# Optimization experiments

Hardware: AMD Instinct MI355X
Metric: run time of the kernel (lower is better)

## Reference

```python
import jax, jax.numpy as jnp
import numpy as np

LN_EPS = 1e-6  # flax nn.LayerNorm default epsilon
NEG_SLOPE = 0.01  # jax.nn.leaky_relu default


def _layer_norm(x, scale, bias):
    m = jnp.mean(x, axis=-1, keepdims=True)
    v = jnp.mean(jnp.square(x - m), axis=-1, keepdims=True)
    return (x - m) * jax.lax.rsqrt(v + LN_EPS) * scale + bias


def setup_inputs() -> dict:
    key = jax.random.key(0)
    ks = jax.random.split(key, 10)
    B, D1, D2, OUT = 32768, 1024, 512, 1024
    inp = {
        "x1": jax.random.normal(ks[0], (B, D1), dtype=jnp.float32),
        "x2": jax.random.normal(ks[1], (B, D2), dtype=jnp.float32),
        # LayerNorm params (one per stream)
        "ln_scale1": jnp.ones((D1,), jnp.float32),
        "ln_bias1": jnp.zeros((D1,), jnp.float32),
        "ln_scale2": jnp.ones((D2,), jnp.float32),
        "ln_bias2": jnp.zeros((D2,), jnp.float32),
        # output Dense per stream: Dense(output_size)
        "W_out1": jax.random.normal(ks[2], (D1, OUT), jnp.float32) / np.sqrt(D1),
        "b_out1": jnp.zeros((OUT,), jnp.float32),
        "W_out2": jax.random.normal(ks[3], (D2, OUT), jnp.float32) / np.sqrt(D2),
        "b_out2": jnp.zeros((OUT,), jnp.float32),
        # gate Dense per stream: Dense(gate_size=output_size) for POINTWISE
        "W_g1": jax.random.normal(ks[4], (D1, OUT), jnp.float32) / np.sqrt(D1),
        "b_g1": jnp.zeros((OUT,), jnp.float32),
        "W_g2": jax.random.normal(ks[5], (D2, OUT), jnp.float32) / np.sqrt(D2),
        "b_g2": jnp.zeros((OUT,), jnp.float32),
    }
    return inp


def reference(x1, x2, ln_scale1, ln_bias1, ln_scale2, ln_bias2,
              W_out1, b_out1, W_out2, b_out2,
              W_g1, b_g1, W_g2, b_g2):
    # per-stream: LayerNorm -> leaky_relu -> Dense(output_size); pre-Dense
    # activation is also fed to the gate Dense.
    f1 = jax.nn.leaky_relu(_layer_norm(x1, ln_scale1, ln_bias1), NEG_SLOPE)
    f2 = jax.nn.leaky_relu(_layer_norm(x2, ln_scale2, ln_bias2), NEG_SLOPE)
    out1 = f1 @ W_out1 + b_out1  # [B, OUT]
    out2 = f2 @ W_out2 + b_out2  # [B, OUT]
    # two-stream POINTWISE gate: sum of gate Denses, sigmoid; the original
    # broadcasts gate [B,OUT] over stack([out1,out2]) and sums axis 0,
    # i.e. output = gate * (out1 + out2).
    gate = jax.nn.sigmoid((f1 @ W_g1 + b_g1) + (f2 @ W_g2 + b_g2))
    return gate * (out1 + out2)
```

## Files before the change

### kernel.cpp

```cpp
#include <hip/hip_runtime.h>
#include <hip/hip_bf16.h>
#include <stdint.h>

typedef __bf16 bf16x8 __attribute__((ext_vector_type(8)));
typedef float floatx4 __attribute__((ext_vector_type(4)));

__device__ __forceinline__ ushort f2bf(float f) {
  union { float f; uint32_t u; } v; v.f = f;
  uint32_t r = (v.u + 0x7fffu + ((v.u >> 16) & 1u)) >> 16;
  return (ushort)r;
}

__device__ __forceinline__ void load_lds16(const ushort* g, ushort* l) {
  __builtin_amdgcn_global_load_lds(
      (__attribute__((address_space(1))) void*)g,
      (__attribute__((address_space(3))) void*)l, 16, 0, 0);
}

__global__ __launch_bounds__(256) void ln2_kernel(
    const float* __restrict__ x1, const float* __restrict__ x2,
    const float* __restrict__ sc1p, const float* __restrict__ bi1p,
    const float* __restrict__ sc2p, const float* __restrict__ bi2p,
    ushort* __restrict__ f) {
  const int row = blockIdx.x;
  const int t = threadIdx.x;
  const float4 v1 = ((const float4*)(x1 + (size_t)row * 1024))[t];
  const float2 v2 = ((const float2*)(x2 + (size_t)row * 512))[t];
  float s1 = v1.x + v1.y + v1.z + v1.w;
  float q1 = v1.x * v1.x + v1.y * v1.y + v1.z * v1.z + v1.w * v1.w;
  float s2 = v2.x + v2.y;
  float q2 = v2.x * v2.x + v2.y * v2.y;
#pragma unroll
  for (int o = 32; o > 0; o >>= 1) {
    s1 += __shfl_down(s1, o);
    q1 += __shfl_down(q1, o);
    s2 += __shfl_down(s2, o);
    q2 += __shfl_down(q2, o);
  }
  __shared__ float red[4][4];
  const int wave = t >> 6, lane = t & 63;
  if (lane == 0) { red[0][wave] = s1; red[1][wave] = q1; red[2][wave] = s2; red[3][wave] = q2; }
  __syncthreads();
  s1 = 0.f; q1 = 0.f; s2 = 0.f; q2 = 0.f;
#pragma unroll
  for (int i = 0; i < 4; i++) { s1 += red[0][i]; q1 += red[1][i]; s2 += red[2][i]; q2 += red[3][i]; }
  const float m1 = s1 * (1.0f / 1024.0f);
  const float r1 = rsqrtf(q1 * (1.0f / 1024.0f) - m1 * m1 + 1e-6f);
  const float m2 = s2 * (1.0f / 512.0f);
  const float r2 = rsqrtf(q2 * (1.0f / 512.0f) - m2 * m2 + 1e-6f);
  const float4 sc1 = ((const float4*)sc1p)[t];
  const float4 bi1 = ((const float4*)bi1p)[t];
  const float2 sc2 = ((const float2*)sc2p)[t];
  const float2 bi2 = ((const float2*)bi2p)[t];
  float y0 = (v1.x - m1) * r1 * sc1.x + bi1.x;
  float y1 = (v1.y - m1) * r1 * sc1.y + bi1.y;
  float y2 = (v1.z - m1) * r1 * sc1.z + bi1.z;
  float y3 = (v1.w - m1) * r1 * sc1.w + bi1.w;
  float z0 = (v2.x - m2) * r2 * sc2.x + bi2.x;
  float z1 = (v2.y - m2) * r2 * sc2.y + bi2.y;
  y0 = y0 >= 0.f ? y0 : 0.01f * y0;
  y1 = y1 >= 0.f ? y1 : 0.01f * y1;
  y2 = y2 >= 0.f ? y2 : 0.01f * y2;
  y3 = y3 >= 0.f ? y3 : 0.01f * y3;
  z0 = z0 >= 0.f ? z0 : 0.01f * z0;
  z1 = z1 >= 0.f ? z1 : 0.01f * z1;
  ushort* frow = f + (size_t)row * 1536;
  ushort4 o1; o1.x = f2bf(y0); o1.y = f2bf(y1); o1.z = f2bf(y2); o1.w = f2bf(y3);
  ((ushort4*)frow)[t] = o1;
  ushort2 o2; o2.x = f2bf(z0); o2.y = f2bf(z1);
  ((ushort2*)(frow + 1024))[t] = o2;
}

__global__ __launch_bounds__(256) void wprep_kernel(
    const float* __restrict__ Wo1, const float* __restrict__ Wo2,
    const float* __restrict__ Wg1, const float* __restrict__ Wg2,
    ushort* __restrict__ WT) {
  __shared__ float tile[32][33];
  const int k0 = blockIdx.x * 32;
  const int j0 = blockIdx.y * 32;
  const int s = blockIdx.z;
  const float* Wa = s ? Wg1 : Wo1;
  const float* Wb = s ? Wg2 : Wo2;
  const int tx = threadIdx.x;
  const int ty = threadIdx.y;
#pragma unroll
  for (int r = 0; r < 4; r++) {
    const int k = k0 + ty + 8 * r;
    const float val = (k < 1024) ? Wa[(size_t)k * 1024 + j0 + tx]
                                 : Wb[(size_t)(k - 1024) * 1024 + j0 + tx];
    tile[ty + 8 * r][tx] = val;
  }
  __syncthreads();
#pragma unroll
  for (int r = 0; r < 4; r++) {
    const int j = j0 + ty + 8 * r;
    const int c = j & 63;
    const int n = (j >> 6) * 128 + (c >> 5) * 64 + s * 32 + ((c >> 4) & 1) * 16 + (c & 15);
    WT[(size_t)n * 1536 + k0 + tx] = f2bf(tile[tx][ty + 8 * r]);
  }
}

__global__ __launch_bounds__(256) void gemm_fused(
    const ushort* __restrict__ A,
    const ushort* __restrict__ Bt,
    const float* __restrict__ bo1, const float* __restrict__ bo2,
    const float* __restrict__ bg1, const float* __restrict__ bg2,
    float* __restrict__ out) {
  __shared__ __align__(16) ushort As[128 * 32];
  __shared__ __align__(16) ushort Bs[128 * 32];
  const int nt = blockIdx.x;
  const int mt = blockIdx.y;
  const int tid = threadIdx.x;
  const int wave = tid >> 6, lane = tid & 63;
  const int wr = wave >> 1, wc = wave & 1;
  const int quad = lane >> 4, low = lane & 15;

  const size_t arow0 = (size_t)mt * 128;
  const size_t brow0 = (size_t)nt * 128;

  const int r0 = tid >> 2;
  const int cc = (tid & 3) ^ ((r0 + (tid >> 4)) & 3);
  const ushort* gA = A + (arow0 + r0) * 1536 + cc * 8;
  const ushort* gB = Bt + (brow0 + r0) * 1536 + cc * 8;
  ushort* lA = &As[wave * 512];
  ushort* lB = &Bs[wave * 512];

  const ushort* pA[4];
  const ushort* pB[4];
#pragma unroll
  for (int i = 0; i < 4; i++) {
    const int rA = wr * 64 + i * 16 + low;
    pA[i] = &As[rA * 32 + (quad ^ ((rA + (rA >> 2)) & 3)) * 8];
    const int rB = wc * 64 + i * 16 + low;
    pB[i] = &Bs[rB * 32 + (quad ^ ((rB + (rB >> 2)) & 3)) * 8];
  }

  floatx4 acc[4][4];
#pragma unroll
  for (int i = 0; i < 4; i++)
#pragma unroll
    for (int j = 0; j < 4; j++) acc[i][j] = (floatx4)0.0f;

  for (int kt = 0; kt < 48; kt++) {
    const ushort* a = gA + kt * 32;
    const ushort* b = gB + kt * 32;
    load_lds16(a, lA);
    load_lds16(a + 64 * 1536, lA + 256 * 8);
    load_lds16(b, lB);
    load_lds16(b + 64 * 1536, lB + 256 * 8);
    __syncthreads();
    bf16x8 af[4], bfr[4];
#pragma unroll
    for (int i = 0; i < 4; i++) af[i] = *(const bf16x8*)pA[i];
#pragma unroll
    for (int j = 0; j < 4; j++) bfr[j] = *(const bf16x8*)pB[j];
#pragma unroll
    for (int i = 0; i < 4; i++)
#pragma unroll
      for (int j = 0; j < 4; j++)
        acc[i][j] = __builtin_amdgcn_mfma_f32_16x16x32_bf16(af[i], bfr[j], acc[i][j], 0, 0, 0);
    __syncthreads();
  }

#pragma unroll
  for (int jt = 0; jt < 2; jt++) {
    const int col = nt * 64 + wc * 32 + jt * 16 + low;
    const float bs = bo1[col] + bo2[col];
    const float bgv = bg1[col] + bg2[col];
#pragma unroll
    for (int i = 0; i < 4; i++) {
      const floatx4 S = acc[i][jt];
      const floatx4 G = acc[i][jt + 2];
      const size_t rb = (size_t)mt * 128 + wr * 64 + i * 16 + quad * 4;
#pragma unroll
      for (int r = 0; r < 4; r++) {
        const float sv = S[r] + bs;
        const float gv = G[r] + bgv;
        const float gate = 1.0f / (1.0f + __expf(-gv));
        out[(rb + r) * 1024 + col] = gate * sv;
      }
    }
  }
}

extern "C" void kernel_launch(void* const* d_in, const int* in_sizes, int n_in,
                              void* d_out, int out_size, void* d_ws, size_t ws_size,
                              hipStream_t stream) {
  const float* x1 = (const float*)d_in[0];
  const float* x2 = (const float*)d_in[1];
  const float* ln_s1 = (const float*)d_in[2];
  const float* ln_b1 = (const float*)d_in[3];
  const float* ln_s2 = (const float*)d_in[4];
  const float* ln_b2 = (const float*)d_in[5];
  const float* W_out1 = (const float*)d_in[6];
  const float* b_out1 = (const float*)d_in[7];
  const float* W_out2 = (const float*)d_in[8];
  const float* b_out2 = (const float*)d_in[9];
  const float* W_g1 = (const float*)d_in[10];
  const float* b_g1 = (const float*)d_in[11];
  const float* W_g2 = (const float*)d_in[12];
  const float* b_g2 = (const float*)d_in[13];
  float* out = (float*)d_out;

  ushort* f = (ushort*)d_ws;
  ushort* WT = f + (size_t)32768 * 1536;

  ln2_kernel<<<32768, 256, 0, stream>>>(x1, x2, ln_s1, ln_b1, ln_s2, ln_b2, f);
  wprep_kernel<<<dim3(48, 32, 2), dim3(32, 8), 0, stream>>>(W_out1, W_out2, W_g1, W_g2, WT);
  gemm_fused<<<dim3(16, 256), 256, 0, stream>>>(f, WT, b_out1, b_out2, b_g1, b_g2, out);
}
```

Baseline: 538.5 us.

## Use 256x256 double-buffered GEMM tiles with 8 waves and one-wave-per-row LayerNorm

The GEMM moves from 128x128 tiles with 4 waves and a single LDS buffer to 256x256 tiles with 8 waves, K-steps of 64, and double-buffered LDS. Loads for the next tile are staged between MFMA phases, and the kernel adds barrier and setprio interleaving plus a grid swizzle for L2 reuse. The goal is to overlap global loads with MFMA work and raise arithmetic intensity per LDS byte. The LayerNorm kernel now handles one row per wave with an xor-shuffle reduction, which drops the block-level sync and LDS. In exchange, the GEMM uses 128 KB of LDS and more registers, which may limit occupancy.

```diff
diff --git a/kernel.cpp b/kernel.cpp
--- a/kernel.cpp
+++ b/kernel.cpp
@@ -16,59 +16,68 @@
       (__attribute__((address_space(1))) void*)g,
       (__attribute__((address_space(3))) void*)l, 16, 0, 0);
 }
+
+__device__ __forceinline__ float leaky(float x) { return x >= 0.f ? x : 0.01f * x; }
 
 __global__ __launch_bounds__(256) void ln2_kernel(
     const float* __restrict__ x1, const float* __restrict__ x2,
     const float* __restrict__ sc1p, const float* __restrict__ bi1p,
     const float* __restrict__ sc2p, const float* __restrict__ bi2p,
     ushort* __restrict__ f) {
-  const int row = blockIdx.x;
-  const int t = threadIdx.x;
-  const float4 v1 = ((const float4*)(x1 + (size_t)row * 1024))[t];
-  const float2 v2 = ((const float2*)(x2 + (size_t)row * 512))[t];
-  float s1 = v1.x + v1.y + v1.z + v1.w;
-  float q1 = v1.x * v1.x + v1.y * v1.y + v1.z * v1.z + v1.w * v1.w;
-  float s2 = v2.x + v2.y;
-  float q2 = v2.x * v2.x + v2.y * v2.y;
-#pragma unroll
-  for (int o = 32; o > 0; o >>= 1) {
-    s1 += __shfl_down(s1, o);
-    q1 += __shfl_down(q1, o);
-    s2 += __shfl_down(s2, o);
-    q2 += __shfl_down(q2, o);
-  }
-  __shared__ float red[4][4];
-  const int wave = t >> 6, lane = t & 63;
-  if (lane == 0) { red[0][wave] = s1; red[1][wave] = q1; red[2][wave] = s2; red[3][wave] = q2; }
-  __syncthreads();
-  s1 = 0.f; q1 = 0.f; s2 = 0.f; q2 = 0.f;
-#pragma unroll
-  for (int i = 0; i < 4; i++) { s1 += red[0][i]; q1 += red[1][i]; s2 += red[2][i]; q2 += red[3][i]; }
+  const int row = (blockIdx.x << 2) + (threadIdx.x >> 6);
+  const int lane = threadIdx.x & 63;
+  const float4* X1 = (const float4*)(x1 + (size_t)row * 1024);
+  const float4* X2 = (const float4*)(x2 + (size_t)row * 512);
+  float4 v1[4], v2[2];
+#pragma unroll
+  for (int j = 0; j < 4; j++) v1[j] = X1[j * 64 + lane];
+#pragma unroll
+  for (int j = 0; j < 2; j++) v2[j] = X2[j * 64 + lane];
+  float s1 = 0.f, q1 = 0.f, s2 = 0.f, q2 = 0.f;
+#pragma unroll
+  for (int j = 0; j < 4; j++) {
+    s1 += v1[j].x + v1[j].y + v1[j].z + v1[j].w;
+    q1 += v1[j].x * v1[j].x + v1[j].y * v1[j].y + v1[j].z * v1[j].z + v1[j].w * v1[j].w;
+  }
+#pragma unroll
+  for (int j = 0; j < 2; j++) {
+    s2 += v2[j].x + v2[j].y + v2[j].z + v2[j].w;
+    q2 += v2[j].x * v2[j].x + v2[j].y * v2[j].y + v2[j].z * v2[j].z + v2[j].w * v2[j].w;
+  }
+#pragma unroll
+  for (int o = 1; o < 64; o <<= 1) {
+    s1 += __shfl_xor(s1, o);
+    q1 += __shfl_xor(q1, o);
+    s2 += __shfl_xor(s2, o);
+    q2 += __shfl_xor(q2, o);
+  }
   const float m1 = s1 * (1.0f / 1024.0f);
   const float r1 = rsqrtf(q1 * (1.0f / 1024.0f) - m1 * m1 + 1e-6f);
   const float m2 = s2 * (1.0f / 512.0f);
   const float r2 = rsqrtf(q2 * (1.0f / 512.0f) - m2 * m2 + 1e-6f);
-  const float4 sc1 = ((const float4*)sc1p)[t];
-  const float4 bi1 = ((const float4*)bi1p)[t];
-  const float2 sc2 = ((const float2*)sc2p)[t];
-  const float2 bi2 = ((const float2*)bi2p)[t];
-  float y0 = (v1.x - m1) * r1 * sc1.x + bi1.x;
-  float y1 = (v1.y - m1) * r1 * sc1.y + bi1.y;
-  float y2 = (v1.z - m1) * r1 * sc1.z + bi1.z;
-  float y3 = (v1.w - m1) * r1 * sc1.w + bi1.w;
-  float z0 = (v2.x - m2) * r2 * sc2.x + bi2.x;
-  float z1 = (v2.y - m2) * r2 * sc2.y + bi2.y;
-  y0 = y0 >= 0.f ? y0 : 0.01f * y0;
-  y1 = y1 >= 0.f ? y1 : 0.01f * y1;
-  y2 = y2 >= 0.f ? y2 : 0.01f * y2;
-  y3 = y3 >= 0.f ? y3 : 0.01f * y3;
-  z0 = z0 >= 0.f ? z0 : 0.01f * z0;
-  z1 = z1 >= 0.f ? z1 : 0.01f * z1;
   ushort* frow = f + (size_t)row * 1536;
-  ushort4 o1; o1.x = f2bf(y0); o1.y = f2bf(y1); o1.z = f2bf(y2); o1.w = f2bf(y3);
-  ((ushort4*)frow)[t] = o1;
-  ushort2 o2; o2.x = f2bf(z0); o2.y = f2bf(z1);
-  ((ushort2*)(frow + 1024))[t] = o2;
+#pragma unroll
+  for (int j = 0; j < 4; j++) {
+    const float4 sc = ((const float4*)sc1p)[j * 64 + lane];
+    const float4 bi = ((const float4*)bi1p)[j * 64 + lane];
+    const float y0 = leaky((v1[j].x - m1) * r1 * sc.x + bi.x);
+    const float y1 = leaky((v1[j].y - m1) * r1 * sc.y + bi.y);
+    const float y2 = leaky((v1[j].z - m1) * r1 * sc.z + bi.z);
+    const float y3 = leaky((v1[j].w - m1) * r1 * sc.w + bi.w);
+    ushort4 o; o.x = f2bf(y0); o.y = f2bf(y1); o.z = f2bf(y2); o.w = f2bf(y3);
+    ((ushort4*)frow)[j * 64 + lane] = o;
+  }
+#pragma unroll
+  for (int j = 0; j < 2; j++) {
+    const float4 sc = ((const float4*)sc2p)[j * 64 + lane];
+    const float4 bi = ((const float4*)bi2p)[j * 64 + lane];
+    const float z0 = leaky((v2[j].x - m2) * r2 * sc.x + bi.x);
+    const float z1 = leaky((v2[j].y - m2) * r2 * sc.y + bi.y);
+    const float z2 = leaky((v2[j].z - m2) * r2 * sc.z + bi.z);
+    const float z3 = leaky((v2[j].w - m2) * r2 * sc.w + bi.w);
+    ushort4 o; o.x = f2bf(z0); o.y = f2bf(z1); o.z = f2bf(z2); o.w = f2bf(z3);
+    ((ushort4*)(frow + 1024))[j * 64 + lane] = o;
+  }
 }
 
 __global__ __launch_bounds__(256) void wprep_kernel(
@@ -100,82 +109,143 @@
   }
 }
 
-__global__ __launch_bounds__(256) void gemm_fused(
+__global__ __launch_bounds__(512, 2) void gemm_fused(
     const ushort* __restrict__ A,
     const ushort* __restrict__ Bt,
     const float* __restrict__ bo1, const float* __restrict__ bo2,
     const float* __restrict__ bg1, const float* __restrict__ bg2,
     float* __restrict__ out) {
-  __shared__ __align__(16) ushort As[128 * 32];
-  __shared__ __align__(16) ushort Bs[128 * 32];
-  const int nt = blockIdx.x;
-  const int mt = blockIdx.y;
+  __shared__ __align__(16) ushort As[2][16384];
+  __shared__ __align__(16) ushort Bs[2][16384];
+  const int orig = blockIdx.x;
+  const int swz = (orig & 7) * 128 + (orig >> 3);
+  const int mt = swz >> 3;
+  const int nt = swz & 7;
   const int tid = threadIdx.x;
   const int wave = tid >> 6, lane = tid & 63;
-  const int wr = wave >> 1, wc = wave & 1;
-  const int quad = lane >> 4, low = lane & 15;
-
-  const size_t arow0 = (size_t)mt * 128;
-  const size_t brow0 = (size_t)nt * 128;
-
-  const int r0 = tid >> 2;
-  const int cc = (tid & 3) ^ ((r0 + (tid >> 4)) & 3);
-  const ushort* gA = A + (arow0 + r0) * 1536 + cc * 8;
-  const ushort* gB = Bt + (brow0 + r0) * 1536 + cc * 8;
-  ushort* lA = &As[wave * 512];
-  ushort* lB = &Bs[wave * 512];
-
-  const ushort* pA[4];
-  const ushort* pB[4];
-#pragma unroll
-  for (int i = 0; i < 4; i++) {
-    const int rA = wr * 64 + i * 16 + low;
-    pA[i] = &As[rA * 32 + (quad ^ ((rA + (rA >> 2)) & 3)) * 8];
-    const int rB = wc * 64 + i * 16 + low;
-    pB[i] = &Bs[rB * 32 + (quad ^ ((rB + (rB >> 2)) & 3)) * 8];
-  }
-
-  floatx4 acc[4][4];
-#pragma unroll
-  for (int i = 0; i < 4; i++)
-#pragma unroll
-    for (int j = 0; j < 4; j++) acc[i][j] = (floatx4)0.0f;
-
-  for (int kt = 0; kt < 48; kt++) {
-    const ushort* a = gA + kt * 32;
-    const ushort* b = gB + kt * 32;
-    load_lds16(a, lA);
-    load_lds16(a + 64 * 1536, lA + 256 * 8);
-    load_lds16(b, lB);
-    load_lds16(b + 64 * 1536, lB + 256 * 8);
-    __syncthreads();
-    bf16x8 af[4], bfr[4];
-#pragma unroll
-    for (int i = 0; i < 4; i++) af[i] = *(const bf16x8*)pA[i];
-#pragma unroll
-    for (int j = 0; j < 4; j++) bfr[j] = *(const bf16x8*)pB[j];
-#pragma unroll
-    for (int i = 0; i < 4; i++)
-#pragma unroll
-      for (int j = 0; j < 4; j++)
-        acc[i][j] = __builtin_amdgcn_mfma_f32_16x16x32_bf16(af[i], bfr[j], acc[i][j], 0, 0, 0);
-    __syncthreads();
-  }
-
-#pragma unroll
-  for (int jt = 0; jt < 2; jt++) {
-    const int col = nt * 64 + wc * 32 + jt * 16 + low;
+  const int wr = wave >> 2, wcol = wave & 3;
+  const int low = lane & 15, quad = lane >> 4;
+
+  const int srow = wave * 8 + (lane >> 3);
+  const int schunk = (lane & 7) ^ (lane >> 3);
+  const ushort* gA0 = A + ((size_t)mt * 256 + srow) * 1536 + schunk * 8;
+  const ushort* gB0 = Bt + ((size_t)nt * 256 + srow) * 1536 + schunk * 8;
+
+  const int q2 = quad ^ (low & 3);
+  const int kx = (low >> 2) & 1;
+  const int offA_k0 = (wr * 128 + low) * 64 + (q2 + 4 * kx) * 8;
+  const int offA_k1 = (wr * 128 + low) * 64 + (q2 + 4 * (1 - kx)) * 8;
+  const int offB_k0 = (wcol * 64 + low) * 64 + (q2 + 4 * kx) * 8;
+  const int offB_k1 = (wcol * 64 + low) * 64 + (q2 + 4 * (1 - kx)) * 8;
+
+  floatx4 acc[8][4];
+#pragma unroll
+  for (int m = 0; m < 8; m++)
+#pragma unroll
+    for (int n = 0; n < 4; n++) acc[m][n] = (floatx4)0.0f;
+
+#define STAGE_A(BUF, KT) do { \
+    const ushort* s_ = gA0 + (KT) * 64; \
+    ushort* d_ = &As[BUF][wave * 512]; \
+    load_lds16(s_, d_); \
+    load_lds16(s_ + 64 * 1536, d_ + 4096); \
+    load_lds16(s_ + 128 * 1536, d_ + 8192); \
+    load_lds16(s_ + 192 * 1536, d_ + 12288); \
+  } while (0)
+#define STAGE_B(BUF, KT) do { \
+    const ushort* s_ = gB0 + (KT) * 64; \
+    ushort* d_ = &Bs[BUF][wave * 512]; \
+    load_lds16(s_, d_); \
+    load_lds16(s_ + 64 * 1536, d_ + 4096); \
+    load_lds16(s_ + 128 * 1536, d_ + 8192); \
+    load_lds16(s_ + 192 * 1536, d_ + 12288); \
+  } while (0)
+
+  STAGE_A(0, 0);
+  STAGE_B(0, 0);
+  asm volatile("s_waitcnt vmcnt(0)" ::: "memory");
+  __builtin_amdgcn_s_barrier();
+  asm volatile("" ::: "memory");
+
+#define TILE_STEP(CUR, T) do { \
+    const ushort* Ac = &As[CUR][0]; \
+    const ushort* Bc = &Bs[CUR][0]; \
+    const bool pf = (T) < 23; \
+    bf16x8 a[4], b[4]; \
+     \
+    _Pragma("unroll") for (int m = 0; m < 4; m++) a[m] = *(const bf16x8*)(Ac + offA_k0 + m * 1024); \
+    _Pragma("unroll") for (int n = 0; n < 4; n++) b[n] = *(const bf16x8*)(Bc + offB_k0 + n * 1024); \
+    if (pf) STAGE_A((CUR) ^ 1, (T) + 1); \
+    asm volatile("" ::: "memory"); \
+    __builtin_amdgcn_s_barrier(); \
+    __builtin_amdgcn_s_setprio(1); \
+    _Pragma("unroll") for (int m = 0; m < 4; m++) \
+      _Pragma("unroll") for (int n = 0; n < 4; n++) \
+        acc[m][n] = __builtin_amdgcn_mfma_f32_16x16x32_bf16(a[m], b[n], acc[m][n], 0, 0, 0); \
+    __builtin_amdgcn_s_setprio(0); \
+    asm volatile("" ::: "memory"); \
+    __builtin_amdgcn_s_barrier(); \
+     \
+    _Pragma("unroll") for (int m = 0; m < 4; m++) a[m] = *(const bf16x8*)(Ac + offA_k0 + (m + 4) * 1024); \
+    if (pf) STAGE_B((CUR) ^ 1, (T) + 1); \
+    asm volatile("" ::: "memory"); \
+    __builtin_amdgcn_s_barrier(); \
+    __builtin_amdgcn_s_setprio(1); \
+    _Pragma("unroll") for (int m = 0; m < 4; m++) \
+      _Pragma("unroll") for (int n = 0; n < 4; n++) \
+        acc[m + 4][n] = __builtin_amdgcn_mfma_f32_16x16x32_bf16(a[m], b[n], acc[m + 4][n], 0, 0, 0); \
+    __builtin_amdgcn_s_setprio(0); \
+    asm volatile("" ::: "memory"); \
+    __builtin_amdgcn_s_barrier(); \
+     \
+    _Pragma("unroll") for (int m = 0; m < 4; m++) a[m] = *(const bf16x8*)(Ac + offA_k1 + m * 1024); \
+    _Pragma("unroll") for (int n = 0; n < 4; n++) b[n] = *(const bf16x8*)(Bc + offB_k1 + n * 1024); \
+    asm volatile("" ::: "memory"); \
+    __builtin_amdgcn_s_barrier(); \
+    __builtin_amdgcn_s_setprio(1); \
+    _Pragma("unroll") for (int m = 0; m < 4; m++) \
+      _Pragma("unroll") for (int n = 0; n < 4; n++) \
+        acc[m][n] = __builtin_amdgcn_mfma_f32_16x16x32_bf16(a[m], b[n], acc[m][n], 0, 0, 0); \
+    __builtin_amdgcn_s_setprio(0); \
+    asm volatile("" ::: "memory"); \
+    __builtin_amdgcn_s_barrier(); \
+     \
+    _Pragma("unroll") for (int m = 0; m < 4; m++) a[m] = *(const bf16x8*)(Ac + offA_k1 + (m + 4) * 1024); \
+    asm volatile("" ::: "memory"); \
+    __builtin_amdgcn_s_barrier(); \
+    __builtin_amdgcn_s_setprio(1); \
+    _Pragma("unroll") for (int m = 0; m < 4; m++) \
+      _Pragma("unroll") for (int n = 0; n < 4; n++) \
+        acc[m + 4][n] = __builtin_amdgcn_mfma_f32_16x16x32_bf16(a[m], b[n], acc[m + 4][n], 0, 0, 0); \
+    __builtin_amdgcn_s_setprio(0); \
+    asm volatile("s_waitcnt vmcnt(0)" ::: "memory"); \
+    __builtin_amdgcn_s_barrier(); \
+    asm volatile("" ::: "memory"); \
+  } while (0)
+
+  for (int tt = 0; tt < 12; tt++) {
+    TILE_STEP(0, 2 * tt);
+    TILE_STEP(1, 2 * tt + 1);
+  }
+#undef TILE_STEP
+#undef STAGE_A
+#undef STAGE_B
+
+  const int colbase = (nt * 4 + wcol) << 5;
+#pragma unroll
+  for (int n = 0; n < 2; n++) {
+    const int col = colbase + n * 16 + low;
     const float bs = bo1[col] + bo2[col];
-    const float bgv = bg1[col] + bg2[col];
-#pragma unroll
-    for (int i = 0; i < 4; i++) {
-      const floatx4 S = acc[i][jt];
-      const floatx4 G = acc[i][jt + 2];
-      const size_t rb = (size_t)mt * 128 + wr * 64 + i * 16 + quad * 4;
+    const float bg = bg1[col] + bg2[col];
+#pragma unroll
+    for (int m = 0; m < 8; m++) {
+      const floatx4 S = acc[m][n];
+      const floatx4 G = acc[m][n + 2];
+      const size_t rb = (size_t)mt * 256 + wr * 128 + m * 16 + quad * 4;
 #pragma unroll
       for (int r = 0; r < 4; r++) {
         const float sv = S[r] + bs;
-        const float gv = G[r] + bgv;
+        const float gv = G[r] + bg;
         const float gate = 1.0f / (1.0f + __expf(-gv));
         out[(rb + r) * 1024 + col] = gate * sv;
       }
@@ -205,7 +275,7 @@
   ushort* f = (ushort*)d_ws;
   ushort* WT = f + (size_t)32768 * 1536;
 
-  ln2_kernel<<<32768, 256, 0, stream>>>(x1, x2, ln_s1, ln_b1, ln_s2, ln_b2, f);
+  ln2_kernel<<<8192, 256, 0, stream>>>(x1, x2, ln_s1, ln_b1, ln_s2, ln_b2, f);
   wprep_kernel<<<dim3(48, 32, 2), dim3(32, 8), 0, stream>>>(W_out1, W_out2, W_g1, W_g2, WT);
-  gemm_fused<<<dim3(16, 256), 256, 0, stream>>>(f, WT, b_out1, b_out2, b_g1, b_g2, out);
-}
+  gemm_fused<<<dim3(1024), dim3(512), 0, stream>>>(f, WT, b_out1, b_out2, b_g1, b_g2, out);
+}
```

New measurement: 517.2 us. -3.9%, faster.
